# Performance work log

Measured on AMD Instinct MI355X. Metric: run time of the kernel, lower is better.

The kernel has to match this reference:

```python
import jax, jax.numpy as jnp
import numpy as np
from functools import partial

STRIDES = (8, 16, 32)
SIZES = ((80, 80), (40, 40), (20, 20))
NUM_CLASSES = 80
NMS_THR = 0.65
SCORE_THR = 0.01
MAX_DET = 100  # fixed-size NMS output (padded; validity = scores > 0)


def setup_inputs() -> dict:
    key = jax.random.key(0)
    ks = jax.random.split(key, 9)
    B = 32
    out = {}
    for i, (h, w) in enumerate(SIZES):
        out[f"cls{i}"] = jax.random.normal(ks[3 * i], (B, NUM_CLASSES, h, w), jnp.float32)
        out[f"reg{i}"] = jax.random.normal(ks[3 * i + 1], (B, 4, h, w), jnp.float32)
        out[f"obj{i}"] = jax.random.normal(ks[3 * i + 2], (B, 1, h, w), jnp.float32)
    return out


def _grid_points():
    # MlvlPointGenerator.grid_priors(with_stride=True), offset=0: (x, y, stride, stride)
    pts = []
    for (h, w), s in zip(SIZES, STRIDES):
        xs = jnp.arange(w, dtype=jnp.float32) * s
        ys = jnp.arange(h, dtype=jnp.float32) * s
        xx, yy = jnp.meshgrid(xs, ys)  # [h, w], x varies fastest -> matches NHWC flatten
        st = jnp.full((h * w,), float(s), jnp.float32)
        pts.append(jnp.stack([xx.ravel(), yy.ravel(), st, st], axis=-1))
    return jnp.concatenate(pts, axis=0)  # [A, 4]


def _flatten(t, c):
    # [N, C, H, W] -> [N, H*W, C]  (permute(0,2,3,1).reshape)
    return t.transpose(0, 2, 3, 1).reshape(t.shape[0], -1, c)


def _decode(points, reg):
    # YOLOXBBoxDecoder: center = pred_xy * stride + point, wh = exp(pred_wh) * stride
    stride = points[:, 2:]                       # [A, 2]
    xys = reg[..., :2] * stride + points[:, :2]  # [B, A, 2]
    whs = jnp.exp(reg[..., 2:]) * stride         # [B, A, 2]
    return jnp.concatenate([xys - whs * 0.5, xys + whs * 0.5], axis=-1)  # x1y1x2y2


def _iou_one_vs_all(b, boxes):
    # b: [4], boxes: [A, 4]
    tl = jnp.maximum(b[:2], boxes[:, :2])
    br = jnp.minimum(b[2:], boxes[:, 2:])
    wh = jnp.clip(br - tl, 0.0)
    inter = wh[:, 0] * wh[:, 1]
    a1 = (b[2] - b[0]) * (b[3] - b[1])
    a2 = (boxes[:, 2] - boxes[:, 0]) * (boxes[:, 3] - boxes[:, 1])
    return inter / (a1 + a2 - inter + 1e-6)


def _nms_image(boxes, cls_scores, objectness):
    # boxes [A,4], cls_scores [A,C] (post-sigmoid), objectness [A] (post-sigmoid)
    max_scores = jnp.max(cls_scores, axis=1)
    labels = jnp.argmax(cls_scores, axis=1)
    scores = max_scores * objectness
    live = jnp.where(scores >= SCORE_THR, scores, -jnp.inf)  # score_thr filter

    # batched_nms: offset boxes per class so boxes of different labels never overlap
    offset = jax.lax.stop_gradient(jnp.max(jnp.abs(boxes)) + 1.0)
    boxes_off = jax.lax.stop_gradient(boxes) + labels.astype(boxes.dtype)[:, None] * offset

    def body(i, state):
        live, keep, kscores = state
        best = jnp.argmax(live)
        kscores = kscores.at[i].set(live[best])
        keep = keep.at[i].set(best)
        iou = _iou_one_vs_all(boxes_off[best], boxes_off)
        live = jnp.where(iou > NMS_THR, -jnp.inf, live)
        live = live.at[best].set(-jnp.inf)
        return live, keep, kscores

    keep0 = jnp.zeros((MAX_DET,), jnp.int32)
    ks0 = jnp.full((MAX_DET,), -jnp.inf, boxes.dtype)
    _, keep, kscores = jax.lax.fori_loop(0, MAX_DET, body, (live, keep0, ks0))

    valid = kscores > -jnp.inf
    out_boxes = jnp.where(valid[:, None], boxes[keep], 0.0)
    out_scores = jnp.where(valid, scores[keep], 0.0)
    out_labels = jnp.where(valid, labels[keep], -1)
    return out_boxes, out_scores, out_labels, valid


def _forward(cls0, cls1, cls2, reg0, reg1, reg2, obj0, obj1, obj2):
    B = cls0.shape[0]
    flat_cls = jax.nn.sigmoid(jnp.concatenate([_flatten(c, NUM_CLASSES) for c in (cls0, cls1, cls2)], axis=1))
    flat_reg = jnp.concatenate([_flatten(r, 4) for r in (reg0, reg1, reg2)], axis=1)
    flat_obj = jax.nn.sigmoid(jnp.concatenate([_flatten(o, 1) for o in (obj0, obj1, obj2)], axis=1))[..., 0]
    points = _grid_points()
    boxes = _decode(points, flat_reg)  # [B, A, 4]
    return jax.vmap(_nms_image)(boxes, flat_cls, flat_obj)


@jax.jit
def reference(cls0, cls1, cls2, reg0, reg1, reg2, obj0, obj1, obj2):
    return _forward(cls0, cls1, cls2, reg0, reg1, reg2, obj0, obj1, obj2)
```

## Files before the change

### kernel.cpp

```cpp
#include <hip/hip_runtime.h>
#include <cmath>

typedef unsigned int uint;
typedef unsigned long long ull;

#define BATCH 32
#define NA 8400
#define NC 80
#define MAXDET 100
#define NMSTHR 0.65f
#define SCTHR 0.01f
#define NEG_INF (-INFINITY)

#define NT 1024
#define NW (NT / 64)
#define EPT 9
#define NBINS 4096
#define CAP 512

__device__ __forceinline__ float stable_sigmoid(float x) {
    if (x >= 0.f) return 1.f / (1.f + expf(-x));
    float e = expf(x);
    return e / (1.f + e);
}

template<int HW, int W, int S>
__device__ __forceinline__ void decode4(
    const float* __restrict__ cls, const float* __restrict__ reg,
    const float* __restrict__ obj, int b, int p, int q, int ag,
    float4* __restrict__ wboxes, int* __restrict__ wlabels, uint* __restrict__ wkeys)
{
    const float* cbase = cls + (size_t)b * NC * HW + (size_t)(q * 20) * HW + p;
    float v[20];
    #pragma unroll
    for (int i = 0; i < 20; ++i) v[i] = cbase[(size_t)i * HW];
    float m = v[0]; int c = 0;
    #pragma unroll
    for (int i = 1; i < 20; ++i)
        if (v[i] > m) { m = v[i]; c = i; }
    c += q * 20;

    #pragma unroll
    for (int o = 1; o <= 2; o <<= 1) {
        float om = __shfl_xor(m, o);
        int   oc = __shfl_xor(c, o);
        if (om > m || (om == m && oc < c)) { m = om; c = oc; }
    }

    if (q == 0) {
        const float* rb = reg + (size_t)b * 4 * HW + p;
        float r0 = rb[0];
        float r1 = rb[HW];
        float r2 = rb[2 * (size_t)HW];
        float r3 = rb[3 * (size_t)HW];
        float ov = obj[(size_t)b * HW + p];

        int y = p / W;
        int x = p - y * W;
        float sc = stable_sigmoid(m) * stable_sigmoid(ov);
        float cx = r0 * (float)S + (float)x * (float)S;
        float cy = r1 * (float)S + (float)y * (float)S;
        float bw = expf(r2) * (float)S;
        float bh = expf(r3) * (float)S;

        wboxes[ag]  = make_float4(cx - bw * 0.5f, cy - bh * 0.5f,
                                  cx + bw * 0.5f, cy + bh * 0.5f);
        wlabels[ag] = c;
        wkeys[ag]   = (sc >= SCTHR) ? ~__float_as_uint(sc) : 0xFFFFFFFFu;
    }
}

__global__ __launch_bounds__(256) void decode_kernel(
    const float* __restrict__ cls0, const float* __restrict__ reg0, const float* __restrict__ obj0,
    const float* __restrict__ cls1, const float* __restrict__ reg1, const float* __restrict__ obj1,
    const float* __restrict__ cls2, const float* __restrict__ reg2, const float* __restrict__ obj2,
    float4* __restrict__ wboxes, int* __restrict__ wlabels, uint* __restrict__ wkeys)
{
    int gid = blockIdx.x * blockDim.x + threadIdx.x;
    int ag = gid >> 2;
    int q  = gid & 3;
    int b = ag / NA;
    int j = ag - b * NA;

    if (j < 6400)
        decode4<6400, 80, 8>(cls0, reg0, obj0, b, j, q, ag, wboxes, wlabels, wkeys);
    else if (j < 8000)
        decode4<1600, 40, 16>(cls1, reg1, obj1, b, j - 6400, q, ag, wboxes, wlabels, wkeys);
    else
        decode4<400, 20, 32>(cls2, reg2, obj2, b, j - 8000, q, ag, wboxes, wlabels, wkeys);
}

__global__ __launch_bounds__(NT) void nms_kernel(
    const float4* __restrict__ wboxes, const int* __restrict__ wlabels,
    const uint* __restrict__ wkeys, float* __restrict__ out)
{
    int b = blockIdx.x;
    int t = threadIdx.x;
    int lane = t & 63;
    int wv = t >> 6;
    const float4* boxes  = wboxes  + (size_t)b * NA;
    const int*    labels = wlabels + (size_t)b * NA;
    const uint*   keys   = wkeys   + (size_t)b * NA;

    __shared__ uint   s_hist[NBINS];
    __shared__ uint   s_cum[NBINS + 1];
    __shared__ uint   s_wsum[NW];
    __shared__ ull    s_skey[CAP];
    __shared__ float4 s_cbox[CAP];
    __shared__ float  s_ca[CAP];
    __shared__ int    s_clb[CAP];
    __shared__ float  s_kbox[MAXDET][4];
    __shared__ float  s_ka1[MAXDET];
    __shared__ int    s_kidx[MAXDET];
    __shared__ float  s_kscr[MAXDET];
    __shared__ int    s_klab[MAXDET];
    __shared__ float  s_red[NW];
    __shared__ float  s_off;
    __shared__ int    s_kept, s_winlo, s_winhi, s_nsel;

    float m = 0.f;
    #pragma unroll
    for (int w = 0; w < EPT; ++w) {
        int e = t + w * NT;
        if (e < NA) {
            float4 v = boxes[e];
            m = fmaxf(m, fmaxf(fmaxf(fabsf(v.x), fabsf(v.y)),
                               fmaxf(fabsf(v.z), fabsf(v.w))));
        }
    }
    #pragma unroll
    for (int o = 32; o >= 1; o >>= 1) m = fmaxf(m, __shfl_xor(m, o));
    if (lane == 0) s_red[wv] = m;
    for (int i = t; i < NBINS; i += NT) s_hist[i] = 0;
    if (t == 0) { s_kept = 0; s_winlo = 0; }
    __syncthreads();
    if (t == 0) {
        float mm = 0.f;
        for (int w = 0; w < NW; ++w) mm = fmaxf(mm, s_red[w]);
        s_off = mm + 1.f;
    }
    #pragma unroll
    for (int w = 0; w < EPT; ++w) {
        int e = t + w * NT;
        if (e < NA) {
            uint k = keys[e];
            if (k != 0xFFFFFFFFu) atomicAdd(&s_hist[k >> 20], 1u);
        }
    }
    __syncthreads();
    float off = s_off;

    uint l0 = s_hist[4 * t], l1 = s_hist[4 * t + 1],
         l2 = s_hist[4 * t + 2], l3 = s_hist[4 * t + 3];
    uint L = l0 + l1 + l2 + l3;
    uint ls = L;
    #pragma unroll
    for (int o = 1; o < 64; o <<= 1) {
        uint v = __shfl_up(ls, o);
        if (lane >= o) ls += v;
    }
    if (lane == 63) s_wsum[wv] = ls;
    __syncthreads();
    if (t < NW) {
        uint v = s_wsum[t];
        uint vs = v;
        #pragma unroll
        for (int o = 1; o < NW; o <<= 1) {
            uint u = __shfl_up(vs, o);
            if ((t & 63) >= o) vs += u;
        }
        s_wsum[t] = vs - v;
    }
    __syncthreads();
    uint base = s_wsum[wv] + (ls - L);
    s_cum[4 * t]     = base;
    s_cum[4 * t + 1] = base + l0;
    s_cum[4 * t + 2] = base + l0 + l1;
    s_cum[4 * t + 3] = base + l0 + l1 + l2;
    if (t == NT - 1) s_cum[NBINS] = base + L;

    for (;;) {
        __syncthreads();
        int kept = s_kept, winlo = s_winlo;
        uint remaining = s_cum[NBINS] - s_cum[winlo];
        if (kept >= MAXDET || winlo >= NBINS || remaining == 0u) break;
        if (t == 0) { s_winhi = winlo + 1; s_nsel = 0; }
        if (t < CAP) s_skey[t] = ~0ull;
        __syncthreads();
        uint cl = s_cum[winlo];
        #pragma unroll
        for (int q = 0; q < 4; ++q) {
            int i = t + q * NT;
            if (i >= winlo && i < NBINS) {
                bool p0 = (s_cum[i + 1] - cl) <= (uint)CAP;
                bool p1 = (i + 1 < NBINS) && ((s_cum[i + 2] - cl) <= (uint)CAP);
                if (p0 && !p1) s_winhi = i + 1;
            }
        }
        __syncthreads();
        int winhi = s_winhi;

        #pragma unroll
        for (int w = 0; w < EPT; ++w) {
            int e = t + w * NT;
            bool q = false;
            uint k = 0;
            if (e < NA) {
                k = keys[e];
                if (k != 0xFFFFFFFFu) {
                    int bin = (int)(k >> 20);
                    q = (bin >= winlo && bin < winhi);
                }
            }
            ull mask = __ballot(q);
            if (mask) {
                int leader = __ffsll(mask) - 1;
                int pbase = 0;
                if (lane == leader) pbase = atomicAdd(&s_nsel, __popcll(mask));
                pbase = __shfl(pbase, leader);
                if (q) {
                    int pos = pbase + __popcll(mask & ((1ull << lane) - 1ull));
                    if (pos < CAP) s_skey[pos] = ((ull)k << 32) | (uint)e;
                }
            }
        }
        __syncthreads();
        int nsel = s_nsel; if (nsel > CAP) nsel = CAP;

        ull k = (t < CAP) ? s_skey[t] : ~0ull;
        for (int k2 = 2; k2 <= CAP; k2 <<= 1) {
            for (int j = k2 >> 1; j > 0; j >>= 1) {
                if (j >= 64) {
                    if (t < CAP) s_skey[t] = k;
                    __syncthreads();
                    if (t < CAP) {
                        ull kp = s_skey[t ^ j];
                        bool low = (t & j) == 0;
                        bool up  = (t & k2) == 0;
                        k = ((k < kp) == (low == up)) ? k : kp;
                    }
                    __syncthreads();
                } else if (t < CAP) {
                    ull kp = __shfl_xor(k, j);
                    bool low = (t & j) == 0;
                    bool up  = (t & k2) == 0;
                    k = ((k < kp) == (low == up)) ? k : kp;
                }
            }
        }
        if (t < CAP) s_skey[t] = k;
        __syncthreads();

        if (t < nsel) {
            ull sk = s_skey[t];
            if (sk != ~0ull) {
                int idx = (int)(sk & 0xFFFFFFFFull);
                float4 rb = boxes[idx];
                int lb = labels[idx];
                float lo = (float)lb * off;
                float c0 = rb.x + lo, c1 = rb.y + lo;
                float c2 = rb.z + lo, c3 = rb.w + lo;
                s_cbox[t] = make_float4(c0, c1, c2, c3);
                s_ca[t]   = (c2 - c0) * (c3 - c1);
                s_clb[t]  = lb;
            }
        }
        __syncthreads();

        if (t < 64) {
            int kept2 = s_kept;
            for (int cb = 0; cb < nsel && kept2 < MAXDET; cb += 64) {
                int ci = cb + lane;
                ull sk = (ci < nsel) ? s_skey[ci] : ~0ull;
                bool has = (sk != ~0ull);
                int idx = 0, lab = 0;
                float sc = 0.f, c0 = 0.f, c1 = 0.f, c2 = 0.f, c3 = 0.f, ca = 0.f;
                if (has) {
                    idx = (int)(sk & 0xFFFFFFFFull);
                    sc  = __uint_as_float(~(uint)(sk >> 32));
                    float4 cbx = s_cbox[ci];
                    c0 = cbx.x; c1 = cbx.y; c2 = cbx.z; c3 = cbx.w;
                    ca = s_ca[ci];
                    lab = s_clb[ci];
                    for (int q = 0; q < kept2; ++q) {
                        float tlx = fmaxf(s_kbox[q][0], c0);
                        float tly = fmaxf(s_kbox[q][1], c1);
                        float brx = fminf(s_kbox[q][2], c2);
                        float bry = fminf(s_kbox[q][3], c3);
                        float ww = fmaxf(brx - tlx, 0.f);
                        float hh = fmaxf(bry - tly, 0.f);
                        float inter = ww * hh;
                        float iou = inter / (s_ka1[q] + ca - inter + 1e-6f);
                        if (iou > NMSTHR) { has = false; break; }
                    }
                }
                ull am = __ballot(has);
                while (am && kept2 < MAXDET) {
                    int f = __ffsll(am) - 1;
                    float f0 = __shfl(c0, f), f1 = __shfl(c1, f);
                    float f2 = __shfl(c2, f), f3 = __shfl(c3, f);
                    float fa = __shfl(ca, f);
                    int   fidx = __shfl(idx, f);
                    int   flab = __shfl(lab, f);
                    float fsc  = __shfl(sc, f);
                    if (lane == 0) {
                        s_kbox[kept2][0] = f0; s_kbox[kept2][1] = f1;
                        s_kbox[kept2][2] = f2; s_kbox[kept2][3] = f3;
                        s_ka1[kept2] = fa; s_kidx[kept2] = fidx;
                        s_kscr[kept2] = fsc; s_klab[kept2] = flab;
                    }
                    kept2++;
                    if (lane == f) has = false;
                    if (has) {
                        float tlx = fmaxf(f0, c0), tly = fmaxf(f1, c1);
                        float brx = fminf(f2, c2), bry = fminf(f3, c3);
                        float ww = fmaxf(brx - tlx, 0.f), hh = fmaxf(bry - tly, 0.f);
                        float inter = ww * hh;
                        float iou = inter / (fa + ca - inter + 1e-6f);
                        if (iou > NMSTHR) has = false;
                    }
                    am = __ballot(has);
                }
            }
            if (lane == 0) s_kept = kept2;
        }
        __syncthreads();
        if (t == 0) s_winlo = s_winhi;
    }
    __syncthreads();

    if (t < MAXDET) {
        int kept = s_kept;
        float4 obx = make_float4(0.f, 0.f, 0.f, 0.f);
        float osc = 0.f, olab = -1.f, oval = 0.f;
        if (t < kept) {
            int idx = s_kidx[t];
            obx  = boxes[idx];
            osc  = s_kscr[t];
            olab = (float)s_klab[t];
            oval = 1.f;
        }
        float* ob = out + ((size_t)b * MAXDET + t) * 4;
        ob[0] = obx.x; ob[1] = obx.y; ob[2] = obx.z; ob[3] = obx.w;
        out[BATCH * MAXDET * 4 + b * MAXDET + t] = osc;
        out[BATCH * MAXDET * 5 + b * MAXDET + t] = olab;
        out[BATCH * MAXDET * 6 + b * MAXDET + t] = oval;
    }
}

extern "C" void kernel_launch(void* const* d_in, const int* in_sizes, int n_in,
                              void* d_out, int out_size, void* d_ws, size_t ws_size,
                              hipStream_t stream) {
    const float* cls0 = (const float*)d_in[0];
    const float* reg0 = (const float*)d_in[1];
    const float* obj0 = (const float*)d_in[2];
    const float* cls1 = (const float*)d_in[3];
    const float* reg1 = (const float*)d_in[4];
    const float* obj1 = (const float*)d_in[5];
    const float* cls2 = (const float*)d_in[6];
    const float* reg2 = (const float*)d_in[7];
    const float* obj2 = (const float*)d_in[8];

    char* ws = (char*)d_ws;
    size_t nBA = (size_t)BATCH * NA;
    float4* wboxes  = (float4*)ws;
    int*    wlabels = (int*)(ws + nBA * 16);
    uint*   wkeys   = (uint*)(ws + nBA * 20);

    int total = BATCH * NA * 4;
    decode_kernel<<<total / 256, 256, 0, stream>>>(
        cls0, reg0, obj0, cls1, reg1, obj1, cls2, reg2, obj2,
        wboxes, wlabels, wkeys);

    nms_kernel<<<BATCH, NT, 0, stream>>>(wboxes, wlabels, wkeys, (float*)d_out);
}
```

Before: 172.6 us.

## Replace serial wave-level greedy NMS with parallel IoU bitmask plus bit-scan selection

Each candidate window now gets a pairwise suppression bitmask built by all 16 waves in parallel, plus a parallel check against boxes already kept. A single wave then walks the alive bitmask with a min-reduction to pick survivors greedily. Before, one wave did serial IoU loops and per-survivor shuffles. The histogram is also fused into the max-abs pass, and its shared memory is aliased with the mask array. In exchange the kernel computes the full upper-triangular IoU matrix even when few survivors are needed, and uses `winhi` where the old code read `s_winhi`.

After: 223.2 us. +29.3%, slower.

```diff
diff --git a/kernel.cpp b/kernel.cpp
--- a/kernel.cpp
+++ b/kernel.cpp
@@ -10,7 +10,6 @@
 #define MAXDET 100
 #define NMSTHR 0.65f
 #define SCTHR 0.01f
-#define NEG_INF (-INFINITY)
 
 #define NT 1024
 #define NW (NT / 64)
@@ -102,22 +101,25 @@
     const int*    labels = wlabels + (size_t)b * NA;
     const uint*   keys   = wkeys   + (size_t)b * NA;
 
-    __shared__ uint   s_hist[NBINS];
+    __shared__ ull    s_mask[CAP][8];
     __shared__ uint   s_cum[NBINS + 1];
-    __shared__ uint   s_wsum[NW];
     __shared__ ull    s_skey[CAP];
     __shared__ float4 s_cbox[CAP];
-    __shared__ float  s_ca[CAP];
-    __shared__ int    s_clb[CAP];
     __shared__ float  s_kbox[MAXDET][4];
-    __shared__ float  s_ka1[MAXDET];
     __shared__ int    s_kidx[MAXDET];
     __shared__ float  s_kscr[MAXDET];
-    __shared__ int    s_klab[MAXDET];
+    __shared__ int    s_kci[MAXDET];
+    __shared__ ull    s_alive[8];
+    __shared__ uint   s_wsum[NW];
     __shared__ float  s_red[NW];
     __shared__ float  s_off;
     __shared__ int    s_kept, s_winlo, s_winhi, s_nsel;
 
+    uint* s_hist = reinterpret_cast<uint*>(&s_mask[0][0]);
+
+    for (int i = t; i < NBINS; i += NT) s_hist[i] = 0;
+    if (t == 0) { s_kept = 0; s_winlo = 0; }
+    __syncthreads();
     float m = 0.f;
     #pragma unroll
     for (int w = 0; w < EPT; ++w) {
@@ -126,29 +128,19 @@
             float4 v = boxes[e];
             m = fmaxf(m, fmaxf(fmaxf(fabsf(v.x), fabsf(v.y)),
                                fmaxf(fabsf(v.z), fabsf(v.w))));
+            uint k = keys[e];
+            if (k != 0xFFFFFFFFu) atomicAdd(&s_hist[k >> 20], 1u);
         }
     }
     #pragma unroll
     for (int o = 32; o >= 1; o >>= 1) m = fmaxf(m, __shfl_xor(m, o));
     if (lane == 0) s_red[wv] = m;
-    for (int i = t; i < NBINS; i += NT) s_hist[i] = 0;
-    if (t == 0) { s_kept = 0; s_winlo = 0; }
     __syncthreads();
     if (t == 0) {
         float mm = 0.f;
         for (int w = 0; w < NW; ++w) mm = fmaxf(mm, s_red[w]);
         s_off = mm + 1.f;
     }
-    #pragma unroll
-    for (int w = 0; w < EPT; ++w) {
-        int e = t + w * NT;
-        if (e < NA) {
-            uint k = keys[e];
-            if (k != 0xFFFFFFFFu) atomicAdd(&s_hist[k >> 20], 1u);
-        }
-    }
-    __syncthreads();
-    float off = s_off;
 
     uint l0 = s_hist[4 * t], l1 = s_hist[4 * t + 1],
          l2 = s_hist[4 * t + 2], l3 = s_hist[4 * t + 3];
@@ -251,81 +243,101 @@
         if (t < CAP) s_skey[t] = k;
         __syncthreads();
 
+        float off = s_off;
         if (t < nsel) {
             ull sk = s_skey[t];
-            if (sk != ~0ull) {
-                int idx = (int)(sk & 0xFFFFFFFFull);
-                float4 rb = boxes[idx];
-                int lb = labels[idx];
-                float lo = (float)lb * off;
-                float c0 = rb.x + lo, c1 = rb.y + lo;
-                float c2 = rb.z + lo, c3 = rb.w + lo;
-                s_cbox[t] = make_float4(c0, c1, c2, c3);
-                s_ca[t]   = (c2 - c0) * (c3 - c1);
-                s_clb[t]  = lb;
+            int idx = (int)(sk & 0xFFFFFFFFull);
+            float4 rb = boxes[idx];
+            float lo = (float)labels[idx] * off;
+            s_cbox[t] = make_float4(rb.x + lo, rb.y + lo, rb.z + lo, rb.w + lo);
+        }
+        __syncthreads();
+
+        int kprev = s_kept;
+
+        bool al = false;
+        if (t < nsel) {
+            al = true;
+            float4 bt = s_cbox[t];
+            float at = (bt.z - bt.x) * (bt.w - bt.y);
+            for (int q = 0; q < kprev; ++q) {
+                float k0 = s_kbox[q][0], k1 = s_kbox[q][1];
+                float k2c = s_kbox[q][2], k3 = s_kbox[q][3];
+                float ak = (k2c - k0) * (k3 - k1);
+                float tlx = fmaxf(k0, bt.x), tly = fmaxf(k1, bt.y);
+                float brx = fminf(k2c, bt.z), bry = fminf(k3, bt.w);
+                float ww = fmaxf(brx - tlx, 0.f), hh = fmaxf(bry - tly, 0.f);
+                float inter = ww * hh;
+                float iou = inter / (ak + at - inter + 1e-6f);
+                if (iou > NMSTHR) { al = false; break; }
+            }
+        }
+        if (wv < 8) {
+            ull bm = __ballot(al);
+            if (lane == 0) s_alive[wv] = bm;
+        }
+
+        for (int i = wv; i < nsel; i += NW) {
+            float4 bi = s_cbox[i];
+            float ai = (bi.z - bi.x) * (bi.w - bi.y);
+            int cb0 = i >> 6;
+            for (int cblk = cb0; cblk < 8; ++cblk) {
+                int j = (cblk << 6) + lane;
+                bool sup = false;
+                if (j > i && j < nsel) {
+                    float4 bj = s_cbox[j];
+                    float aj = (bj.z - bj.x) * (bj.w - bj.y);
+                    float tlx = fmaxf(bi.x, bj.x), tly = fmaxf(bi.y, bj.y);
+                    float brx = fminf(bi.z, bj.z), bry = fminf(bi.w, bj.w);
+                    float ww = fmaxf(brx - tlx, 0.f), hh = fmaxf(bry - tly, 0.f);
+                    float inter = ww * hh;
+                    float iou = inter / (ai + aj - inter + 1e-6f);
+                    sup = iou > NMSTHR;
+                }
+                ull bm = __ballot(sup);
+                if (lane == 0) s_mask[i][cblk] = bm;
             }
         }
         __syncthreads();
 
         if (t < 64) {
             int kept2 = s_kept;
-            for (int cb = 0; cb < nsel && kept2 < MAXDET; cb += 64) {
-                int ci = cb + lane;
-                ull sk = (ci < nsel) ? s_skey[ci] : ~0ull;
-                bool has = (sk != ~0ull);
-                int idx = 0, lab = 0;
-                float sc = 0.f, c0 = 0.f, c1 = 0.f, c2 = 0.f, c3 = 0.f, ca = 0.f;
-                if (has) {
-                    idx = (int)(sk & 0xFFFFFFFFull);
-                    sc  = __uint_as_float(~(uint)(sk >> 32));
-                    float4 cbx = s_cbox[ci];
-                    c0 = cbx.x; c1 = cbx.y; c2 = cbx.z; c3 = cbx.w;
-                    ca = s_ca[ci];
-                    lab = s_clb[ci];
-                    for (int q = 0; q < kept2; ++q) {
-                        float tlx = fmaxf(s_kbox[q][0], c0);
-                        float tly = fmaxf(s_kbox[q][1], c1);
-                        float brx = fminf(s_kbox[q][2], c2);
-                        float bry = fminf(s_kbox[q][3], c3);
-                        float ww = fmaxf(brx - tlx, 0.f);
-                        float hh = fmaxf(bry - tly, 0.f);
-                        float inter = ww * hh;
-                        float iou = inter / (s_ka1[q] + ca - inter + 1e-6f);
-                        if (iou > NMSTHR) { has = false; break; }
-                    }
-                }
-                ull am = __ballot(has);
-                while (am && kept2 < MAXDET) {
-                    int f = __ffsll(am) - 1;
-                    float f0 = __shfl(c0, f), f1 = __shfl(c1, f);
-                    float f2 = __shfl(c2, f), f3 = __shfl(c3, f);
-                    float fa = __shfl(ca, f);
-                    int   fidx = __shfl(idx, f);
-                    int   flab = __shfl(lab, f);
-                    float fsc  = __shfl(sc, f);
-                    if (lane == 0) {
-                        s_kbox[kept2][0] = f0; s_kbox[kept2][1] = f1;
-                        s_kbox[kept2][2] = f2; s_kbox[kept2][3] = f3;
-                        s_ka1[kept2] = fa; s_kidx[kept2] = fidx;
-                        s_kscr[kept2] = fsc; s_klab[kept2] = flab;
-                    }
-                    kept2++;
-                    if (lane == f) has = false;
-                    if (has) {
-                        float tlx = fmaxf(f0, c0), tly = fmaxf(f1, c1);
-                        float brx = fminf(f2, c2), bry = fminf(f3, c3);
-                        float ww = fmaxf(brx - tlx, 0.f), hh = fmaxf(bry - tly, 0.f);
-                        float inter = ww * hh;
-                        float iou = inter / (fa + ca - inter + 1e-6f);
-                        if (iou > NMSTHR) has = false;
-                    }
-                    am = __ballot(has);
-                }
+            ull alive = (lane < 8) ? s_alive[lane] : 0ull;
+            while (kept2 < MAXDET) {
+                int pos = (alive != 0ull) ? ((lane << 6) + __ffsll(alive) - 1)
+                                          : 0x7FFFFFFF;
+                #pragma unroll
+                for (int o = 1; o <= 32; o <<= 1) {
+                    int op = __shfl_xor(pos, o);
+                    pos = (op < pos) ? op : pos;
+                }
+                if (pos == 0x7FFFFFFF) break;
+                int i = pos;
+                if (lane == 0) {
+                    ull sk = s_skey[i];
+                    s_kidx[kept2] = (int)(sk & 0xFFFFFFFFull);
+                    s_kscr[kept2] = __uint_as_float(~(uint)(sk >> 32));
+                    s_kci[kept2]  = i;
+                }
+                if (lane < 8) {
+                    alive &= ~s_mask[i][lane];
+                    if ((i >> 6) == lane) alive &= ~(1ull << (i & 63));
+                }
+                kept2++;
             }
             if (lane == 0) s_kept = kept2;
         }
         __syncthreads();
-        if (t == 0) s_winlo = s_winhi;
+
+        {
+            int kept2 = s_kept;
+            if (t >= kprev && t < kept2) {
+                float4 cb = s_cbox[s_kci[t]];
+                s_kbox[t][0] = cb.x; s_kbox[t][1] = cb.y;
+                s_kbox[t][2] = cb.z; s_kbox[t][3] = cb.w;
+            }
+        }
+        if (t == 0) s_winlo = winhi;
     }
     __syncthreads();
 
@@ -337,7 +349,7 @@
             int idx = s_kidx[t];
             obx  = boxes[idx];
             osc  = s_kscr[t];
-            olab = (float)s_klab[t];
+            olab = (float)labels[idx];
             oval = 1.f;
         }
         float* ob = out + ((size_t)b * MAXDET + t) * 4;
```
